# Optimization experiments

Hardware: AMD Instinct MI355X
Metric: run time of the kernel (lower is better)

The kernel has to match this reference:

```python
import jax, jax.numpy as jnp
import numpy as np

N = 50000
E = 800000
D_IN, D_HID, D_OUT = 256, 256, 128


def _xavier(key, shape):
    fan_in, fan_out = shape
    limit = float(np.sqrt(6.0 / (fan_in + fan_out)))
    return jax.random.uniform(key, shape, jnp.float32, -limit, limit)


def setup_inputs() -> dict:
    key = jax.random.key(0)
    ks = jax.random.split(key, 12)
    x = jax.random.normal(ks[0], (N, D_IN), jnp.float32)
    edge_index = jax.random.randint(ks[1], (2, E), 0, N, dtype=jnp.int64)
    batch = jnp.zeros((N,), jnp.int64)
    # per-layer: message weight W, linear weight LW (stored [in, out]), bias b
    w1 = _xavier(ks[2], (D_IN, D_HID))
    lw1 = _xavier(ks[3], (D_IN, D_HID))
    lb1 = jnp.zeros((D_HID,), jnp.float32)
    w2 = _xavier(ks[4], (D_HID, D_HID))
    lw2 = _xavier(ks[5], (D_HID, D_HID))
    lb2 = jnp.zeros((D_HID,), jnp.float32)
    w3 = _xavier(ks[6], (D_HID, D_OUT))
    lw3 = _xavier(ks[7], (D_HID, D_OUT))
    lb3 = jnp.zeros((D_OUT,), jnp.float32)
    return {"x": x, "edge_index": edge_index, "batch": batch,
            "w1": w1, "lw1": lw1, "lb1": lb1,
            "w2": w2, "lw2": lw2, "lb2": lb2,
            "w3": w3, "lw3": lw3, "lb3": lb3}


def _gcn_layer(x, W, LW, b, row, col, norm):
    # message: norm * (x_j @ W); equivalent and cheaper: transform nodes once, gather
    xw = x @ W                                   # [N, out]
    msg = norm[:, None] * xw[row]                # [E, out]
    agg = jax.ops.segment_sum(msg, col, num_segments=x.shape[0])  # scatter-add at col
    return agg + x @ LW + b                      # residual linear path


def reference(x, edge_index, batch, w1, lw1, lb1, w2, lw2, lb2, w3, lw3, lb3):
    row, col = edge_index[0], edge_index[1]
    ones = jnp.ones((row.shape[0],), x.dtype)
    out_deg = jax.ops.segment_sum(ones, row, num_segments=N)
    in_deg = jax.ops.segment_sum(ones, col, num_segments=N)
    # inf at zero-degree nodes never gets gathered (those nodes have no edges)
    norm = out_deg[row] ** -0.5 * in_deg[col] ** -0.5  # [E]

    h = jax.nn.relu(_gcn_layer(x, w1, lw1, lb1, row, col, norm))
    h = jax.nn.relu(_gcn_layer(h, w2, lw2, lb2, row, col, norm))
    h = jax.nn.sigmoid(_gcn_layer(h, w3, lw3, lb3, row, col, norm))
    return h
```

## Files before the change

### kernel.cpp

```cpp
#include <hip/hip_runtime.h>
#include <hip/hip_bf16.h>
#include <math.h>

#define NNODES 50000
#define NEDGES 800000
#define HNB 128
#define HBINS 50176
#define SCAN_NB 196

typedef short s8v __attribute__((ext_vector_type(8)));
typedef float f4v __attribute__((ext_vector_type(4)));
using bf16 = __hip_bfloat16;

static __device__ __forceinline__ float bflo(unsigned int x) {
    union { unsigned int i; float f; } c; c.i = x << 16; return c.f;
}
static __device__ __forceinline__ float bfhi(unsigned int x) {
    union { unsigned int i; float f; } c; c.i = x & 0xffff0000u; return c.f;
}


__global__ void k_packb(const float* __restrict__ W, const float* __restrict__ LW,
                        bf16* __restrict__ out, int K, int C) {
    int i = blockIdx.x * blockDim.x + threadIdx.x;
    int C2 = 2 * C;
    if (i >= K * C2) return;
    int k = i / C2, j = i % C2;
    float v = (j < C) ? W[k * C + j] : LW[k * C + (j - C)];
    out[i] = __float2bfloat16(v);
}


__global__ __launch_bounds__(256) void k_hist(const int* __restrict__ ei, ushort* __restrict__ partials) {
    __shared__ unsigned int h32[HBINS / 2];
    int b = blockIdx.x, row = blockIdx.y, t = threadIdx.x;
    for (int i = t; i < HBINS / 2; i += 256) h32[i] = 0;
    __syncthreads();
    const int chunk = NEDGES / HNB;
    int beg = b * chunk, end = beg + chunk;
    const int* p = ei + (size_t)row * NEDGES;
    for (int e = beg + t; e < end; e += 256) {
        int id = p[e];
        atomicAdd(&h32[id >> 1], 1u << (16 * (id & 1)));
    }
    __syncthreads();
    unsigned int* o32 = (unsigned int*)(partials + ((size_t)row * HNB + b) * HBINS);
    for (int i = t; i < HBINS / 2; i += 256) o32[i] = h32[i];
}

__global__ __launch_bounds__(256) void k_hist_reduce(const ushort* __restrict__ partials,
                                                     float* __restrict__ rsqrt_out,
                                                     int* __restrict__ in_cnt,
                                                     int* __restrict__ block_sums) {
    __shared__ int sm[256];
    int row = blockIdx.y;
    int i = blockIdx.x * 256 + threadIdx.x;
    const ushort* p = partials + (size_t)row * HNB * HBINS + i;
    int s = 0;
#pragma unroll 4
    for (int b = 0; b < HNB; ++b) s += p[(size_t)b * HBINS];
    if (row == 0) {
        if (i < NNODES) rsqrt_out[i] = rsqrtf((float)s);
    } else {
        if (i < NNODES) in_cnt[i] = s;
        sm[threadIdx.x] = s;
        __syncthreads();
        for (int off = 128; off > 0; off >>= 1) {
            if (threadIdx.x < off) sm[threadIdx.x] += sm[threadIdx.x + off];
            __syncthreads();
        }
        if (threadIdx.x == 0) block_sums[blockIdx.x] = sm[0];
    }
}


__global__ void k_scan_blocks(const int* __restrict__ block_sums, int* __restrict__ block_base, int nb) {
    __shared__ int s[256];
    int t = threadIdx.x;
    int v = (t < nb) ? block_sums[t] : 0;
    s[t] = v;
    __syncthreads();
    for (int off = 1; off < 256; off <<= 1) {
        int u = (t >= off) ? s[t - off] : 0;
        __syncthreads();
        s[t] += u;
        __syncthreads();
    }
    block_base[t] = s[t] - v;
}

__global__ void k_scan_final(const int* __restrict__ in_cnt, const int* __restrict__ block_base,
                             int* __restrict__ offsets, int* __restrict__ cursor) {
    __shared__ int s[256];
    int b = blockIdx.x, t = threadIdx.x;
    int i = b * 256 + t;
    int v = (i < NNODES) ? in_cnt[i] : 0;
    s[t] = v;
    __syncthreads();
    for (int off = 1; off < 256; off <<= 1) {
        int u = (t >= off) ? s[t - off] : 0;
        __syncthreads();
        s[t] += u;
        __syncthreads();
    }
    int excl = s[t] - v + block_base[b];
    if (i < NNODES) { offsets[i] = excl; cursor[i] = excl; }
    if (i == NNODES - 1) offsets[NNODES] = excl + v;
}

__global__ void k_scatter(const int* __restrict__ ei, int* __restrict__ cursor,
                          int* __restrict__ src_sorted) {
    int e = blockIdx.x * blockDim.x + threadIdx.x;
    if (e < NEDGES) {
        int r = ei[e], c = ei[NEDGES + e];
        int p = atomicAdd(&cursor[c], 1);
        src_sorted[p] = r;
    }
}

template<int D, int C2, int ACT>
__global__ __launch_bounds__(64) void k_agg_fused(const bf16* __restrict__ xwcat,
                                                  const int* __restrict__ offsets,
                                                  const int* __restrict__ src_sorted,
                                                  const float* __restrict__ rsqrt_out,
                                                  const float* __restrict__ bias,
                                                  void* __restrict__ out) {
    const int L = D / 8;
    const int G = 64 / L;
    const int U = 4;
    int lane = threadIdx.x;
    int v = blockIdx.x;
    int g = lane / L, sl = lane % L;

    int beg = offsets[v], end = offsets[v + 1];
    int deg = end - beg;
    int dcap = min(deg, 64);

    int id = 0; float wl = 0.f;
    if (lane < dcap) {
        id = src_sorted[beg + lane];
        wl = rsqrt_out[id];
    }

    float acc[U][8];
#pragma unroll
    for (int u = 0; u < U; ++u)
#pragma unroll
        for (int c = 0; c < 8; ++c) acc[u][c] = 0.f;

    const ushort* base = (const ushort*)xwcat + sl * 8;

    for (int e0 = 0; e0 < dcap; e0 += G * U) {
#pragma unroll
        for (int u = 0; u < U; ++u) {
            int e = e0 + u * G + g;
            int s = __shfl(id, e & 63, 64);
            float w = __shfl(wl, e & 63, 64);
            if (e >= dcap) w = 0.f;
            uint4 q = *(const uint4*)(base + (size_t)s * C2);
            acc[u][0] += w * bflo(q.x); acc[u][1] += w * bfhi(q.x);
            acc[u][2] += w * bflo(q.y); acc[u][3] += w * bfhi(q.y);
            acc[u][4] += w * bflo(q.z); acc[u][5] += w * bfhi(q.z);
            acc[u][6] += w * bflo(q.w); acc[u][7] += w * bfhi(q.w);
        }
    }
    for (int j = beg + 64 + g; j < end; j += G) {
        int s = src_sorted[j];
        float w = rsqrt_out[s];
        uint4 q = *(const uint4*)(base + (size_t)s * C2);
        acc[0][0] += w * bflo(q.x); acc[0][1] += w * bfhi(q.x);
        acc[0][2] += w * bflo(q.y); acc[0][3] += w * bfhi(q.y);
        acc[0][4] += w * bflo(q.z); acc[0][5] += w * bfhi(q.z);
        acc[0][6] += w * bflo(q.w); acc[0][7] += w * bfhi(q.w);
    }

#pragma unroll
    for (int c = 0; c < 8; ++c) acc[0][c] = (acc[0][c] + acc[1][c]) + (acc[2][c] + acc[3][c]);
#pragma unroll
    for (int d = 32; d >= L; d >>= 1) {
#pragma unroll
        for (int c = 0; c < 8; ++c) acc[0][c] += __shfl_down(acc[0][c], d, 64);
    }

    if (lane < L) {
        float sc = (deg > 0) ? rsqrtf((float)deg) : 0.f;
        const ushort* lwp = (const ushort*)xwcat + (size_t)v * C2 + D + sl * 8;
        uint4 ql = *(const uint4*)lwp;
        const float* bp = bias + sl * 8;
        float4 b0 = *(const float4*)bp, b1 = *(const float4*)(bp + 4);
        float h[8];
        h[0] = acc[0][0] * sc + bflo(ql.x) + b0.x;
        h[1] = acc[0][1] * sc + bfhi(ql.x) + b0.y;
        h[2] = acc[0][2] * sc + bflo(ql.y) + b0.z;
        h[3] = acc[0][3] * sc + bfhi(ql.y) + b0.w;
        h[4] = acc[0][4] * sc + bflo(ql.z) + b1.x;
        h[5] = acc[0][5] * sc + bfhi(ql.z) + b1.y;
        h[6] = acc[0][6] * sc + bflo(ql.w) + b1.z;
        h[7] = acc[0][7] * sc + bfhi(ql.w) + b1.w;
        if (ACT == 1) {
            union { bf16 hh[8]; uint4 u; } o;
#pragma unroll
            for (int c = 0; c < 8; ++c) o.hh[c] = __float2bfloat16(fmaxf(h[c], 0.f));
            *(uint4*)((ushort*)out + (size_t)v * D + sl * 8) = o.u;
        } else {
            float r[8];
#pragma unroll
            for (int c = 0; c < 8; ++c) r[c] = 1.f / (1.f + expf(-h[c]));
            float* op = (float*)out + (size_t)v * D + sl * 8;
            *(float4*)op = (float4){r[0], r[1], r[2], r[3]};
            *(float4*)(op + 4) = (float4){r[4], r[5], r[6], r[7]};
        }
    }
}

template<int C2, bool A_BF16>
__global__ __launch_bounds__(256) void k_gemm_fused(const void* __restrict__ Aptr,
                                                    const bf16* __restrict__ B,
                                                    bf16* __restrict__ Out) {
    __shared__ bf16 As[64][40];
    __shared__ bf16 Bs[128][40];
    const int R = NNODES;
    int t = threadIdx.x;
    int wave = t >> 6, lane = t & 63;
    int r0 = blockIdx.x * 64;
    int n0 = blockIdx.y * 128;

    f4v acc[8];
#pragma unroll
    for (int i = 0; i < 8; ++i) acc[i] = (f4v){0.f, 0.f, 0.f, 0.f};

    int arow = t >> 2, aseg = t & 3;
    int bn = t & 127, bhalf = t >> 7;

    for (int k0 = 0; k0 < 256; k0 += 32) {
        {
            union { bf16 h[8]; uint4 v; } u;
            int gr = r0 + arow;
            if (gr < R) {
                if (A_BF16) {
                    const bf16* Ab = (const bf16*)Aptr;
                    u.v = *(const uint4*)(Ab + (size_t)gr * 256 + k0 + aseg * 8);
                } else {
                    const float* Af = (const float*)Aptr;
                    const float4* p = (const float4*)(Af + (size_t)gr * 256 + k0 + aseg * 8);
                    float4 f0 = p[0], f1 = p[1];
                    u.h[0] = __float2bfloat16(f0.x); u.h[1] = __float2bfloat16(f0.y);
                    u.h[2] = __float2bfloat16(f0.z); u.h[3] = __float2bfloat16(f0.w);
                    u.h[4] = __float2bfloat16(f1.x); u.h[5] = __float2bfloat16(f1.y);
                    u.h[6] = __float2bfloat16(f1.z); u.h[7] = __float2bfloat16(f1.w);
                }
            } else {
                u.v = (uint4){0, 0, 0, 0};
            }
            *(uint4*)&As[arow][aseg * 8] = u.v;
        }
        {
#pragma unroll
            for (int s8 = 0; s8 < 2; ++s8) {
                int kseg = bhalf * 2 + s8;
                union { bf16 h[8]; uint4 v; } u;
#pragma unroll
                for (int j = 0; j < 8; ++j)
                    u.h[j] = B[(size_t)(k0 + kseg * 8 + j) * C2 + n0 + bn];
                *(uint4*)&Bs[bn][kseg * 8] = u.v;
            }
        }
        __syncthreads();
        int m = wave * 16 + (lane & 15);
        int kq = (lane >> 4) * 8;
        s8v a = *(const s8v*)&As[m][kq];
#pragma unroll
        for (int nt = 0; nt < 8; ++nt) {
            s8v b = *(const s8v*)&Bs[nt * 16 + (lane & 15)][kq];
            acc[nt] = __builtin_amdgcn_mfma_f32_16x16x32_bf16(a, b, acc[nt], 0, 0, 0);
        }
        __syncthreads();
    }
#pragma unroll
    for (int nt = 0; nt < 8; ++nt) {
#pragma unroll
        for (int r = 0; r < 4; ++r) {
            int grow = r0 + wave * 16 + (lane >> 4) * 4 + r;
            int gcol = n0 + nt * 16 + (lane & 15);
            if (grow < R)
                Out[(size_t)grow * C2 + gcol] = __float2bfloat16(acc[nt][r]);
        }
    }
}


extern "C" void kernel_launch(void* const* d_in, const int* in_sizes, int n_in,
                              void* d_out, int out_size, void* d_ws, size_t ws_size,
                              hipStream_t stream) {
    const float* x   = (const float*)d_in[0];
    const int*   ei  = (const int*)d_in[1];
    const float* w1  = (const float*)d_in[3];
    const float* lw1 = (const float*)d_in[4];
    const float* lb1 = (const float*)d_in[5];
    const float* w2  = (const float*)d_in[6];
    const float* lw2 = (const float*)d_in[7];
    const float* lb2 = (const float*)d_in[8];
    const float* w3  = (const float*)d_in[9];
    const float* lw3 = (const float*)d_in[10];
    const float* lb3 = (const float*)d_in[11];
    float* out = (float*)d_out;

    char* ws = (char*)d_ws;
    size_t off = 0;
    auto alloc = [&](size_t bytes) -> void* {
        void* p = ws + off;
        off += (bytes + 255) & ~(size_t)255;
        return p;
    };
    int*    in_cnt     = (int*)alloc((size_t)HBINS * 4);
    float*  rsqrt_out  = (float*)alloc((size_t)HBINS * 4);
    int*    offsets    = (int*)alloc((size_t)(NNODES + 1) * 4);
    int*    cursor     = (int*)alloc((size_t)NNODES * 4);
    int*    block_sums = (int*)alloc((size_t)256 * 4);
    int*    block_base = (int*)alloc((size_t)256 * 4);
    ushort* partials   = (ushort*)alloc((size_t)2 * HNB * HBINS * 2);
    int*    src_sorted = (int*)alloc((size_t)NEDGES * 4);
    bf16*   wcat1      = (bf16*)alloc((size_t)256 * 512 * 2);
    bf16*   wcat2      = (bf16*)alloc((size_t)256 * 512 * 2);
    bf16*   wcat3      = (bf16*)alloc((size_t)256 * 256 * 2);
    bf16*   xwcat      = (bf16*)alloc((size_t)NNODES * 512 * 2);
    bf16*   h1         = (bf16*)alloc((size_t)NNODES * 256 * 2);
    bf16*   h2         = (bf16*)alloc((size_t)NNODES * 256 * 2);

    k_packb<<<512, 256, 0, stream>>>(w1, lw1, wcat1, 256, 256);
    k_packb<<<512, 256, 0, stream>>>(w2, lw2, wcat2, 256, 256);
    k_packb<<<256, 256, 0, stream>>>(w3, lw3, wcat3, 256, 128);

    k_hist<<<dim3(HNB, 2), 256, 0, stream>>>(ei, partials);
    k_hist_reduce<<<dim3(SCAN_NB, 2), 256, 0, stream>>>(partials, rsqrt_out, in_cnt, block_sums);
    k_scan_blocks<<<1, 256, 0, stream>>>(block_sums, block_base, SCAN_NB);
    k_scan_final<<<SCAN_NB, 256, 0, stream>>>(in_cnt, block_base, offsets, cursor);
    int eblocks = (NEDGES + 255) / 256;
    k_scatter<<<eblocks, 256, 0, stream>>>(ei, cursor, src_sorted);

    int gx = (NNODES + 63) / 64;

    k_gemm_fused<512, false><<<dim3(gx, 4), 256, 0, stream>>>(x, wcat1, xwcat);
    k_agg_fused<256, 512, 1><<<NNODES, 64, 0, stream>>>(xwcat, offsets, src_sorted, rsqrt_out, lb1, h1);
    k_gemm_fused<512, true><<<dim3(gx, 4), 256, 0, stream>>>(h1, wcat2, xwcat);
    k_agg_fused<256, 512, 1><<<NNODES, 64, 0, stream>>>(xwcat, offsets, src_sorted, rsqrt_out, lb2, h2);
    k_gemm_fused<256, true><<<dim3(gx, 2), 256, 0, stream>>>(h2, wcat3, xwcat);
    k_agg_fused<128, 256, 2><<<NNODES, 64, 0, stream>>>(xwcat, offsets, src_sorted, rsqrt_out, lb3, out);
}
```

Measured before the change: 440.7 us.

## Retile GEMM to 128x128 with direct LDS loads and split aggregation by column slices

The weights are now packed transposed, so the GEMM B tile can be streamed with global_load_lds 16-byte copies instead of strided scalar gathers. The GEMM tile grows to 128x128 with a 2x2 wave grid, and each wave computes a 4x4 block of MFMA tiles. This raises operand reuse from registers and removes the scalar B gather that was the load bottleneck. The aggregation kernel now puts four nodes in a 256-thread block and splits the feature dimension into 64-column slices across grid.y, giving more concurrent edges per slice. The cost is re-reading the edge list and degree weights once per column slice, plus possible LDS bank conflicts from the unpadded 32-wide tiles.

```diff
diff --git a/kernel.cpp b/kernel.cpp
--- a/kernel.cpp
+++ b/kernel.cpp
@@ -10,6 +10,7 @@
 
 typedef short s8v __attribute__((ext_vector_type(8)));
 typedef float f4v __attribute__((ext_vector_type(4)));
+typedef unsigned int u32;
 using bf16 = __hip_bfloat16;
 
 static __device__ __forceinline__ float bflo(unsigned int x) {
@@ -18,15 +19,19 @@
 static __device__ __forceinline__ float bfhi(unsigned int x) {
     union { unsigned int i; float f; } c; c.i = x & 0xffff0000u; return c.f;
 }
-
-
-__global__ void k_packb(const float* __restrict__ W, const float* __restrict__ LW,
-                        bf16* __restrict__ out, int K, int C) {
+static __device__ __forceinline__ void gld_lds16(const void* g, void* l) {
+    __builtin_amdgcn_global_load_lds((const __attribute__((address_space(1))) u32*)g,
+                                     (__attribute__((address_space(3))) u32*)l, 16, 0, 0);
+}
+
+
+__global__ void k_packbt(const float* __restrict__ W, const float* __restrict__ LW,
+                         bf16* __restrict__ out, int K, int C) {
     int i = blockIdx.x * blockDim.x + threadIdx.x;
     int C2 = 2 * C;
     if (i >= K * C2) return;
-    int k = i / C2, j = i % C2;
-    float v = (j < C) ? W[k * C + j] : LW[k * C + (j - C)];
+    int n = i / K, k = i % K;
+    float v = (n < C) ? W[k * C + n] : LW[k * C + (n - C)];
     out[i] = __float2bfloat16(v);
 }
 
@@ -119,18 +124,18 @@
 }
 
 template<int D, int C2, int ACT>
-__global__ __launch_bounds__(64) void k_agg_fused(const bf16* __restrict__ xwcat,
-                                                  const int* __restrict__ offsets,
-                                                  const int* __restrict__ src_sorted,
-                                                  const float* __restrict__ rsqrt_out,
-                                                  const float* __restrict__ bias,
-                                                  void* __restrict__ out) {
-    const int L = D / 8;
-    const int G = 64 / L;
-    const int U = 4;
-    int lane = threadIdx.x;
-    int v = blockIdx.x;
-    int g = lane / L, sl = lane % L;
+__global__ __launch_bounds__(256) void k_agg_fused(const bf16* __restrict__ xwcat,
+                                                   const int* __restrict__ offsets,
+                                                   const int* __restrict__ src_sorted,
+                                                   const float* __restrict__ rsqrt_out,
+                                                   const float* __restrict__ bias,
+                                                   void* __restrict__ out) {
+    const int U = 2;
+    int lane = threadIdx.x & 63;
+    int v = blockIdx.x * 4 + (threadIdx.x >> 6);
+    if (v >= NNODES) return;
+    int col0 = blockIdx.y * 64;
+    int g = lane >> 3, sl = lane & 7;
 
     int beg = offsets[v], end = offsets[v + 1];
     int deg = end - beg;
@@ -148,12 +153,12 @@
 #pragma unroll
         for (int c = 0; c < 8; ++c) acc[u][c] = 0.f;
 
-    const ushort* base = (const ushort*)xwcat + sl * 8;
-
-    for (int e0 = 0; e0 < dcap; e0 += G * U) {
+    const ushort* base = (const ushort*)xwcat + col0 + sl * 8;
+
+    for (int e0 = 0; e0 < dcap; e0 += 8 * U) {
 #pragma unroll
         for (int u = 0; u < U; ++u) {
-            int e = e0 + u * G + g;
+            int e = e0 + u * 8 + g;
             int s = __shfl(id, e & 63, 64);
             float w = __shfl(wl, e & 63, 64);
             if (e >= dcap) w = 0.f;
@@ -164,7 +169,7 @@
             acc[u][6] += w * bflo(q.w); acc[u][7] += w * bfhi(q.w);
         }
     }
-    for (int j = beg + 64 + g; j < end; j += G) {
+    for (int j = beg + 64 + g; j < end; j += 8) {
         int s = src_sorted[j];
         float w = rsqrt_out[s];
         uint4 q = *(const uint4*)(base + (size_t)s * C2);
@@ -175,18 +180,18 @@
     }
 
 #pragma unroll
-    for (int c = 0; c < 8; ++c) acc[0][c] = (acc[0][c] + acc[1][c]) + (acc[2][c] + acc[3][c]);
-#pragma unroll
-    for (int d = 32; d >= L; d >>= 1) {
+    for (int c = 0; c < 8; ++c) acc[0][c] += acc[1][c];
+#pragma unroll
+    for (int d = 32; d >= 8; d >>= 1) {
 #pragma unroll
         for (int c = 0; c < 8; ++c) acc[0][c] += __shfl_down(acc[0][c], d, 64);
     }
 
-    if (lane < L) {
+    if (lane < 8) {
         float sc = (deg > 0) ? rsqrtf((float)deg) : 0.f;
-        const ushort* lwp = (const ushort*)xwcat + (size_t)v * C2 + D + sl * 8;
+        const ushort* lwp = (const ushort*)xwcat + (size_t)v * C2 + D + col0 + sl * 8;
         uint4 ql = *(const uint4*)lwp;
-        const float* bp = bias + sl * 8;
+        const float* bp = bias + col0 + sl * 8;
         float4 b0 = *(const float4*)bp, b1 = *(const float4*)(bp + 4);
         float h[8];
         h[0] = acc[0][0] * sc + bflo(ql.x) + b0.x;
@@ -201,12 +206,12 @@
             union { bf16 hh[8]; uint4 u; } o;
 #pragma unroll
             for (int c = 0; c < 8; ++c) o.hh[c] = __float2bfloat16(fmaxf(h[c], 0.f));
-            *(uint4*)((ushort*)out + (size_t)v * D + sl * 8) = o.u;
+            *(uint4*)((ushort*)out + (size_t)v * D + col0 + sl * 8) = o.u;
         } else {
             float r[8];
 #pragma unroll
             for (int c = 0; c < 8; ++c) r[c] = 1.f / (1.f + expf(-h[c]));
-            float* op = (float*)out + (size_t)v * D + sl * 8;
+            float* op = (float*)out + (size_t)v * D + col0 + sl * 8;
             *(float4*)op = (float4){r[0], r[1], r[2], r[3]};
             *(float4*)(op + 4) = (float4){r[4], r[5], r[6], r[7]};
         }
@@ -215,75 +220,89 @@
 
 template<int C2, bool A_BF16>
 __global__ __launch_bounds__(256) void k_gemm_fused(const void* __restrict__ Aptr,
-                                                    const bf16* __restrict__ B,
+                                                    const bf16* __restrict__ Bt,
                                                     bf16* __restrict__ Out) {
-    __shared__ bf16 As[64][40];
-    __shared__ bf16 Bs[128][40];
-    const int R = NNODES;
+    __shared__ bf16 As[128 * 32];
+    __shared__ bf16 Bs[128 * 32];
     int t = threadIdx.x;
     int wave = t >> 6, lane = t & 63;
-    int r0 = blockIdx.x * 64;
+    int r0 = blockIdx.x * 128;
     int n0 = blockIdx.y * 128;
-
-    f4v acc[8];
-#pragma unroll
-    for (int i = 0; i < 8; ++i) acc[i] = (f4v){0.f, 0.f, 0.f, 0.f};
-
-    int arow = t >> 2, aseg = t & 3;
-    int bn = t & 127, bhalf = t >> 7;
+    int wr = wave >> 1, wc = wave & 1;
+
+    f4v acc[4][4];
+#pragma unroll
+    for (int i = 0; i < 4; ++i)
+#pragma unroll
+        for (int j = 0; j < 4; ++j) acc[i][j] = (f4v){0.f, 0.f, 0.f, 0.f};
 
     for (int k0 = 0; k0 < 256; k0 += 32) {
-        {
-            union { bf16 h[8]; uint4 v; } u;
-            int gr = r0 + arow;
-            if (gr < R) {
-                if (A_BF16) {
-                    const bf16* Ab = (const bf16*)Aptr;
-                    u.v = *(const uint4*)(Ab + (size_t)gr * 256 + k0 + aseg * 8);
-                } else {
-                    const float* Af = (const float*)Aptr;
-                    const float4* p = (const float4*)(Af + (size_t)gr * 256 + k0 + aseg * 8);
+        if (A_BF16) {
+            const char* Ab = (const char*)Aptr;
+#pragma unroll
+            for (int r = 0; r < 2; ++r) {
+                int o = r * 4096 + wave * 1024 + lane * 16;
+                int row = o >> 6, kb = o & 63;
+                if (r0 + row < NNODES)
+                    gld_lds16(Ab + (size_t)(r0 + row) * 512 + k0 * 2 + kb, (char*)As + o);
+            }
+        } else {
+            const float* Af = (const float*)Aptr;
+#pragma unroll
+            for (int r = 0; r < 2; ++r) {
+                int o = r * 4096 + t * 16;
+                int row = o >> 6, kb = o & 63;
+                union { bf16 h[8]; uint4 v; } u;
+                if (r0 + row < NNODES) {
+                    const float4* p = (const float4*)(Af + (size_t)(r0 + row) * 256 + k0 + kb / 2);
                     float4 f0 = p[0], f1 = p[1];
                     u.h[0] = __float2bfloat16(f0.x); u.h[1] = __float2bfloat16(f0.y);
                     u.h[2] = __float2bfloat16(f0.z); u.h[3] = __float2bfloat16(f0.w);
                     u.h[4] = __float2bfloat16(f1.x); u.h[5] = __float2bfloat16(f1.y);
                     u.h[6] = __float2bfloat16(f1.z); u.h[7] = __float2bfloat16(f1.w);
+                } else {
+                    u.v = (uint4){0, 0, 0, 0};
                 }
-            } else {
-                u.v = (uint4){0, 0, 0, 0};
+                *(uint4*)((char*)As + o) = u.v;
             }
-            *(uint4*)&As[arow][aseg * 8] = u.v;
         }
         {
 #pragma unroll
-            for (int s8 = 0; s8 < 2; ++s8) {
-                int kseg = bhalf * 2 + s8;
-                union { bf16 h[8]; uint4 v; } u;
-#pragma unroll
-                for (int j = 0; j < 8; ++j)
-                    u.h[j] = B[(size_t)(k0 + kseg * 8 + j) * C2 + n0 + bn];
-                *(uint4*)&Bs[bn][kseg * 8] = u.v;
+            for (int r = 0; r < 2; ++r) {
+                int o = r * 4096 + wave * 1024 + lane * 16;
+                int row = o >> 6, kb = o & 63;
+                gld_lds16((const char*)Bt + (size_t)(n0 + row) * 512 + k0 * 2 + kb, (char*)Bs + o);
             }
         }
         __syncthreads();
-        int m = wave * 16 + (lane & 15);
-        int kq = (lane >> 4) * 8;
-        s8v a = *(const s8v*)&As[m][kq];
-#pragma unroll
-        for (int nt = 0; nt < 8; ++nt) {
-            s8v b = *(const s8v*)&Bs[nt * 16 + (lane & 15)][kq];
-            acc[nt] = __builtin_amdgcn_mfma_f32_16x16x32_bf16(a, b, acc[nt], 0, 0, 0);
-        }
-        __syncthreads();
-    }
-#pragma unroll
-    for (int nt = 0; nt < 8; ++nt) {
-#pragma unroll
-        for (int r = 0; r < 4; ++r) {
-            int grow = r0 + wave * 16 + (lane >> 4) * 4 + r;
-            int gcol = n0 + nt * 16 + (lane & 15);
-            if (grow < R)
-                Out[(size_t)grow * C2 + gcol] = __float2bfloat16(acc[nt][r]);
+        int ml = lane & 15, kq = (lane >> 4) * 8;
+        s8v a[4], b[4];
+#pragma unroll
+        for (int i = 0; i < 4; ++i)
+            a[i] = *(const s8v*)&As[(wr * 64 + i * 16 + ml) * 32 + kq];
+#pragma unroll
+        for (int j = 0; j < 4; ++j)
+            b[j] = *(const s8v*)&Bs[(wc * 64 + j * 16 + ml) * 32 + kq];
+#pragma unroll
+        for (int i = 0; i < 4; ++i)
+#pragma unroll
+            for (int j = 0; j < 4; ++j)
+                acc[i][j] = __builtin_amdgcn_mfma_f32_16x16x32_bf16(a[i], b[j], acc[i][j], 0, 0, 0);
+        __syncthreads();
+    }
+    int ml = lane & 15, q4 = (lane >> 4) * 4;
+#pragma unroll
+    for (int i = 0; i < 4; ++i) {
+#pragma unroll
+        for (int rr = 0; rr < 4; ++rr) {
+            int grow = r0 + wr * 64 + i * 16 + q4 + rr;
+            if (grow < NNODES) {
+#pragma unroll
+                for (int j = 0; j < 4; ++j) {
+                    int gcol = n0 + wc * 64 + j * 16 + ml;
+                    Out[(size_t)grow * C2 + gcol] = __float2bfloat16(acc[i][j][rr]);
+                }
+            }
         }
     }
 }
@@ -320,16 +339,16 @@
     int*    block_base = (int*)alloc((size_t)256 * 4);
     ushort* partials   = (ushort*)alloc((size_t)2 * HNB * HBINS * 2);
     int*    src_sorted = (int*)alloc((size_t)NEDGES * 4);
-    bf16*   wcat1      = (bf16*)alloc((size_t)256 * 512 * 2);
-    bf16*   wcat2      = (bf16*)alloc((size_t)256 * 512 * 2);
+    bf16*   wcat1      = (bf16*)alloc((size_t)512 * 256 * 2);
+    bf16*   wcat2      = (bf16*)alloc((size_t)512 * 256 * 2);
     bf16*   wcat3      = (bf16*)alloc((size_t)256 * 256 * 2);
     bf16*   xwcat      = (bf16*)alloc((size_t)NNODES * 512 * 2);
     bf16*   h1         = (bf16*)alloc((size_t)NNODES * 256 * 2);
     bf16*   h2         = (bf16*)alloc((size_t)NNODES * 256 * 2);
 
-    k_packb<<<512, 256, 0, stream>>>(w1, lw1, wcat1, 256, 256);
-    k_packb<<<512, 256, 0, stream>>>(w2, lw2, wcat2, 256, 256);
-    k_packb<<<256, 256, 0, stream>>>(w3, lw3, wcat3, 256, 128);
+    k_packbt<<<512, 256, 0, stream>>>(w1, lw1, wcat1, 256, 256);
+    k_packbt<<<512, 256, 0, stream>>>(w2, lw2, wcat2, 256, 256);
+    k_packbt<<<256, 256, 0, stream>>>(w3, lw3, wcat3, 256, 128);
 
     k_hist<<<dim3(HNB, 2), 256, 0, stream>>>(ei, partials);
     k_hist_reduce<<<dim3(SCAN_NB, 2), 256, 0, stream>>>(partials, rsqrt_out, in_cnt, block_sums);
@@ -338,12 +357,13 @@
     int eblocks = (NEDGES + 255) / 256;
     k_scatter<<<eblocks, 256, 0, stream>>>(ei, cursor, src_sorted);
 
-    int gx = (NNODES + 63) / 64;
+    int gx = (NNODES + 127) / 128;
+    int ax = (NNODES + 3) / 4;
 
     k_gemm_fused<512, false><<<dim3(gx, 4), 256, 0, stream>>>(x, wcat1, xwcat);
-    k_agg_fused<256, 512, 1><<<NNODES, 64, 0, stream>>>(xwcat, offsets, src_sorted, rsqrt_out, lb1, h1);
+    k_agg_fused<256, 512, 1><<<dim3(ax, 4), 256, 0, stream>>>(xwcat, offsets, src_sorted, rsqrt_out, lb1, h1);
     k_gemm_fused<512, true><<<dim3(gx, 4), 256, 0, stream>>>(h1, wcat2, xwcat);
-    k_agg_fused<256, 512, 1><<<NNODES, 64, 0, stream>>>(xwcat, offsets, src_sorted, rsqrt_out, lb2, h2);
+    k_agg_fused<256, 512, 1><<<dim3(ax, 4), 256, 0, stream>>>(xwcat, offsets, src_sorted, rsqrt_out, lb2, h2);
     k_gemm_fused<256, true><<<dim3(gx, 2), 256, 0, stream>>>(h2, wcat3, xwcat);
-    k_agg_fused<128, 256, 2><<<NNODES, 64, 0, stream>>>(xwcat, offsets, src_sorted, rsqrt_out, lb3, out);
-}
+    k_agg_fused<128, 256, 2><<<dim3(ax, 2), 256, 0, stream>>>(xwcat, offsets, src_sorted, rsqrt_out, lb3, out);
+}
```

Measured after the change: 500.8 us. 13.6% more time.
